# Optimization experiments

Hardware: AMD Instinct MI355X
Metric: run time of the kernel (lower is better)

Reference implementation:

```python
import jax, jax.numpy as jnp
import numpy as np


def setup_inputs() -> dict:
    key = jax.random.key(0)
    ks = jax.random.split(key, 8)
    B, M, N, F, H, O = 4, 4096, 4096, 8, 128, 8
    feat = jax.random.normal(ks[0], (B, N, F), dtype=jnp.float32)
    adj = jax.random.uniform(ks[1], (B, M, N), dtype=jnp.float32)
    # MLP params (Linear: y = x @ W.T + b), torch default-like scale
    def lin(k, fan_in, fan_out):
        lim = 1.0 / np.sqrt(fan_in)
        kw, kb = jax.random.split(k)
        W = jax.random.uniform(kw, (fan_out, fan_in), minval=-lim, maxval=lim, dtype=jnp.float32)
        b = jax.random.uniform(kb, (fan_out,), minval=-lim, maxval=lim, dtype=jnp.float32)
        return W, b
    W1, b1 = lin(ks[2], F, H)
    W2, b2 = lin(ks[3], H, H)
    W3, b3 = lin(ks[4], H, O)
    return {"feat": feat, "adj": adj, "W1": W1, "b1": b1, "W2": W2, "b2": b2, "W3": W3, "b3": b3}


def reference(feat, adj, W1, b1, W2, b2, W3, b3):
    # b = sum_n adj[..., m, n] * feat[..., n, f]  ==  adj @ feat
    b = jnp.einsum('bmn,bnf->bmf', adj, feat)  # [B, M, F]
    h = jax.nn.elu(b @ W1.T + b1)              # [B, M, H]
    h = jax.nn.elu(h @ W2.T + b2)              # [B, M, H]
    c = h @ W3.T + b3                          # [B, M, O]
    return c
```

## Files before the change

### kernel.cpp

```cpp
#include <hip/hip_runtime.h>
#include <cstdint>
#include <cstddef>

#define B_ 4
#define M_ 4096
#define N_ 4096
#define F_ 8
#define H_ 128
#define O_ 8

__device__ __forceinline__ uint32_t f2bf1(float x) {
    uint32_t u = __float_as_uint(x);
    return (u + 0x7fffu + ((u >> 16) & 1u)) >> 16;
}

__device__ __forceinline__ void bf8dec(uint4 w, float* f) {
    f[0] = __uint_as_float(w.x << 16);
    f[1] = __uint_as_float(w.x & 0xffff0000u);
    f[2] = __uint_as_float(w.y << 16);
    f[3] = __uint_as_float(w.y & 0xffff0000u);
    f[4] = __uint_as_float(w.z << 16);
    f[5] = __uint_as_float(w.z & 0xffff0000u);
    f[6] = __uint_as_float(w.w << 16);
    f[7] = __uint_as_float(w.w & 0xffff0000u);
}

__device__ __forceinline__ float elu(float x) {
    return x > 0.f ? x : (__expf(x) - 1.f);
}

typedef float vf4_t __attribute__((ext_vector_type(4)));
__device__ __forceinline__ float4 ntload4(const float4* p) {
    vf4_t v = __builtin_nontemporal_load((const vf4_t*)p);
    float4 r;
    r.x = v.x; r.y = v.y; r.z = v.z; r.w = v.w;
    return r;
}

__global__ __launch_bounds__(512, 4)
void k_fused(const float* __restrict__ adj, const float* __restrict__ feat,
             const float* __restrict__ W1, const float* __restrict__ b1,
             const float* __restrict__ W2, const float* __restrict__ b2,
             const float* __restrict__ W3, const float* __restrict__ b3,
             float* __restrict__ out) {
    __shared__ alignas(16) unsigned char smem[65536];
    uint4* sfeat = (uint4*)smem;
    float* sW1 = (float*)smem;
    float* sW3 = (float*)(smem + 4096);
    float* sB1 = (float*)(smem + 8320);
    float* sB2 = (float*)(smem + 8832);
    float* sB3 = (float*)(smem + 9344);
    float* sH  = (float*)(smem + 9376);
    unsigned short* sW2b = (unsigned short*)(smem + 26272);

    const int tid = threadIdx.x;
    const int bb  = blockIdx.x >> 7;
    const int rb  = blockIdx.x & 127;

    const float4* fsrc = (const float4*)(feat + (size_t)bb * (N_ * F_));
    for (int n = tid; n < N_; n += 512) {
        float4 lo = fsrc[2 * n];
        float4 hi = fsrc[2 * n + 1];
        uint4 w;
        w.x = f2bf1(lo.x) | (f2bf1(lo.y) << 16);
        w.y = f2bf1(lo.z) | (f2bf1(lo.w) << 16);
        w.z = f2bf1(hi.x) | (f2bf1(hi.y) << 16);
        w.w = f2bf1(hi.z) | (f2bf1(hi.w) << 16);
        sfeat[(n & 3) * 1024 + (n >> 2)] = w;
    }
    __syncthreads();

    const int lane = tid & 63;
    const int wv   = tid >> 6;
    const int m0   = rb * 32 + wv * 4;

    const float4* arow = (const float4*)(adj + (size_t)(bb * M_ + m0) * N_);

    float acc[4][8];
#pragma unroll
    for (int r = 0; r < 4; ++r)
#pragma unroll
        for (int f = 0; f < 8; ++f) acc[r][f] = 0.f;

    float4 na0 = ntload4(arow + lane);
    float4 na1 = ntload4(arow + lane + 1024);
    float4 na2 = ntload4(arow + lane + 2048);
    float4 na3 = ntload4(arow + lane + 3072);

#pragma unroll 1
    for (int c = 0; c < 16; ++c) {
        const int ni = (c << 6) + lane;
        float4 a0 = na0, a1 = na1, a2 = na2, a3 = na3;
        uint4 w0 = sfeat[ni];
        uint4 w1 = sfeat[1024 + ni];
        uint4 w2 = sfeat[2048 + ni];
        uint4 w3 = sfeat[3072 + ni];
        if (c < 15) {
            const int nn = ni + 64;
            na0 = ntload4(arow + nn);
            na1 = ntload4(arow + nn + 1024);
            na2 = ntload4(arow + nn + 2048);
            na3 = ntload4(arow + nn + 3072);
        }

        float av[4][4] = {{a0.x, a1.x, a2.x, a3.x},
                          {a0.y, a1.y, a2.y, a3.y},
                          {a0.z, a1.z, a2.z, a3.z},
                          {a0.w, a1.w, a2.w, a3.w}};
        uint4 ww[4] = {w0, w1, w2, w3};
#pragma unroll
        for (int k = 0; k < 4; ++k) {
            float f[8];
            bf8dec(ww[k], f);
#pragma unroll
            for (int r = 0; r < 4; ++r) {
                const float a = av[k][r];
#pragma unroll
                for (int j = 0; j < 8; ++j)
                    acc[r][j] = fmaf(a, f[j], acc[r][j]);
            }
        }
    }

#pragma unroll
    for (int r = 0; r < 4; ++r)
#pragma unroll
        for (int j = 0; j < 8; ++j) {
            float v = acc[r][j];
            v += __shfl_xor(v, 32, 64);
            v += __shfl_xor(v, 16, 64);
            v += __shfl_xor(v, 8, 64);
            v += __shfl_xor(v, 4, 64);
            v += __shfl_xor(v, 2, 64);
            v += __shfl_xor(v, 1, 64);
            acc[r][j] = v;
        }

    __syncthreads();

    for (int i = tid; i < H_ * F_ / 4; i += 512)
        ((float4*)sW1)[i] = ((const float4*)W1)[i];

    for (int i8 = tid; i8 < H_ * H_ / 8; i8 += 512) {
        const int idx = i8 * 8;
        const int o = idx >> 7, k = idx & 127;
        float4 lo = ((const float4*)W2)[i8 * 2];
        float4 hi = ((const float4*)W2)[i8 * 2 + 1];
        uint4 w;
        w.x = f2bf1(lo.x) | (f2bf1(lo.y) << 16);
        w.y = f2bf1(lo.z) | (f2bf1(lo.w) << 16);
        w.z = f2bf1(hi.x) | (f2bf1(hi.y) << 16);
        w.w = f2bf1(hi.z) | (f2bf1(hi.w) << 16);
        *((uint4*)&sW2b[o * 136 + k]) = w;
    }

    for (int i = tid; i < O_ * H_ / 4; i += 512) {
        const int idx = i * 4;
        const int o = idx >> 7, k = idx & 127;
        *((float4*)&sW3[o * 132 + k]) = ((const float4*)W3)[i];
    }
    if (tid < H_) { sB1[tid] = b1[tid]; sB2[tid] = b2[tid]; }
    if (tid < O_) sB3[tid] = b3[tid];
    __syncthreads();

    float w1a[8], w1b[8];
    {
        float4 x0 = *(const float4*)&sW1[lane * 8];
        float4 x1 = *(const float4*)&sW1[lane * 8 + 4];
        float4 y0 = *(const float4*)&sW1[(lane + 64) * 8];
        float4 y1 = *(const float4*)&sW1[(lane + 64) * 8 + 4];
        w1a[0]=x0.x; w1a[1]=x0.y; w1a[2]=x0.z; w1a[3]=x0.w;
        w1a[4]=x1.x; w1a[5]=x1.y; w1a[6]=x1.z; w1a[7]=x1.w;
        w1b[0]=y0.x; w1b[1]=y0.y; w1b[2]=y0.z; w1b[3]=y0.w;
        w1b[4]=y1.x; w1b[5]=y1.y; w1b[6]=y1.z; w1b[7]=y1.w;
    }
    const float bias1a = sB1[lane], bias1b = sB1[lane + 64];
#pragma unroll
    for (int r = 0; r < 4; ++r) {
        float t0 = bias1a, t1 = bias1b;
#pragma unroll
        for (int j = 0; j < 8; ++j) {
            t0 = fmaf(acc[r][j], w1a[j], t0);
            t1 = fmaf(acc[r][j], w1b[j], t1);
        }
        sH[(wv * 4 + r) * 132 + lane]      = elu(t0);
        sH[(wv * 4 + r) * 132 + lane + 64] = elu(t1);
    }

    float a20[4], a21[4];
#pragma unroll
    for (int r = 0; r < 4; ++r) { a20[r] = 0.f; a21[r] = 0.f; }
#pragma unroll 1
    for (int oct = 0; oct < 16; ++oct) {
        uint4 wa = *(const uint4*)&sW2b[lane * 136 + (oct << 3)];
        uint4 wb = *(const uint4*)&sW2b[(lane + 64) * 136 + (oct << 3)];
        float A[8], Bv[8];
        bf8dec(wa, A);
        bf8dec(wb, Bv);
#pragma unroll
        for (int r = 0; r < 4; ++r) {
            const float* hp = &sH[(wv * 4 + r) * 132 + (oct << 3)];
            float4 h0 = *(const float4*)hp;
            float4 h1v = *(const float4*)(hp + 4);
            float hv[8] = {h0.x, h0.y, h0.z, h0.w, h1v.x, h1v.y, h1v.z, h1v.w};
#pragma unroll
            for (int j = 0; j < 8; ++j) {
                a20[r] = fmaf(hv[j], A[j], a20[r]);
                a21[r] = fmaf(hv[j], Bv[j], a21[r]);
            }
        }
    }
    const float bias2a = sB2[lane], bias2b = sB2[lane + 64];
#pragma unroll
    for (int r = 0; r < 4; ++r) {
        sH[(wv * 4 + r) * 132 + lane]      = elu(a20[r] + bias2a);
        sH[(wv * 4 + r) * 132 + lane + 64] = elu(a21[r] + bias2b);
    }

    if (lane < 32) {
        const int rr = lane >> 3;
        const int oo = lane & 7;
        const float* hp = &sH[(wv * 4 + rr) * 132];
        const float* wp = &sW3[oo * 132];
        float s = sB3[oo];
#pragma unroll
        for (int k = 0; k < 128; k += 4) {
            float4 h = *(const float4*)(hp + k);
            float4 g = *(const float4*)(wp + k);
            s = fmaf(h.x, g.x, fmaf(h.y, g.y, fmaf(h.z, g.z, fmaf(h.w, g.w, s))));
        }
        out[(size_t)(bb * M_ + m0 + rr) * 8 + oo] = s;
    }
}

extern "C" void kernel_launch(void* const* d_in, const int* in_sizes, int n_in,
                              void* d_out, int out_size, void* d_ws, size_t ws_size,
                              hipStream_t stream) {
    const float* feat = (const float*)d_in[0];
    const float* adj  = (const float*)d_in[1];
    const float* W1   = (const float*)d_in[2];
    const float* b1   = (const float*)d_in[3];
    const float* W2   = (const float*)d_in[4];
    const float* b2   = (const float*)d_in[5];
    const float* W3   = (const float*)d_in[6];
    const float* b3   = (const float*)d_in[7];
    float* outp = (float*)d_out;

    k_fused<<<dim3(B_ * 128), dim3(512), 0, stream>>>(
        adj, feat, W1, b1, W2, b2, W3, b3, outp);
}
```

Baseline: 378.0 us.

## Prefetch MLP weights into registers before reduction and lower occupancy bound

The W1, bias, W2 and W3 global loads are issued right after the adjacency accumulation loop, so their latency overlaps the cross-lane shuffle reduction. W1 and the biases stay in registers instead of going through shared memory. W2 is converted to bf16 in registers and written to shared memory after the existing barrier. The barrier is moved to after the layer-1 sH writes, and launch_bounds is relaxed from 4 to 2 blocks per CU to give room for the extra live registers, which may reduce occupancy in the memory-bound main loop.

```diff
diff --git a/kernel.cpp b/kernel.cpp
--- a/kernel.cpp
+++ b/kernel.cpp
@@ -37,7 +37,7 @@
     return r;
 }
 
-__global__ __launch_bounds__(512, 4)
+__global__ __launch_bounds__(512, 2)
 void k_fused(const float* __restrict__ adj, const float* __restrict__ feat,
              const float* __restrict__ W1, const float* __restrict__ b1,
              const float* __restrict__ W2, const float* __restrict__ b2,
@@ -45,17 +45,16 @@
              float* __restrict__ out) {
     __shared__ alignas(16) unsigned char smem[65536];
     uint4* sfeat = (uint4*)smem;
-    float* sW1 = (float*)smem;
-    float* sW3 = (float*)(smem + 4096);
-    float* sB1 = (float*)(smem + 8320);
-    float* sB2 = (float*)(smem + 8832);
-    float* sB3 = (float*)(smem + 9344);
-    float* sH  = (float*)(smem + 9376);
-    unsigned short* sW2b = (unsigned short*)(smem + 26272);
-
-    const int tid = threadIdx.x;
-    const int bb  = blockIdx.x >> 7;
-    const int rb  = blockIdx.x & 127;
+    float* sW3 = (float*)smem;
+    float* sH  = (float*)(smem + 4224);
+    unsigned short* sW2b = (unsigned short*)(smem + 21120);
+
+    const int tid  = threadIdx.x;
+    const int bb   = blockIdx.x >> 7;
+    const int rb   = blockIdx.x & 127;
+    const int lane = tid & 63;
+    const int wv   = tid >> 6;
+    const int m0   = rb * 32 + wv * 4;
 
     const float4* fsrc = (const float4*)(feat + (size_t)bb * (N_ * F_));
     for (int n = tid; n < N_; n += 512) {
@@ -69,10 +68,6 @@
         sfeat[(n & 3) * 1024 + (n >> 2)] = w;
     }
     __syncthreads();
-
-    const int lane = tid & 63;
-    const int wv   = tid >> 6;
-    const int m0   = rb * 32 + wv * 4;
 
     const float4* arow = (const float4*)(adj + (size_t)(bb * M_ + m0) * N_);
 
@@ -122,6 +117,23 @@
         }
     }
 
+    float4 x0 = *(const float4*)&W1[lane * 8];
+    float4 x1 = *(const float4*)&W1[lane * 8 + 4];
+    float4 y0 = *(const float4*)&W1[(lane + 64) * 8];
+    float4 y1 = *(const float4*)&W1[(lane + 64) * 8 + 4];
+    const float bias1a = b1[lane], bias1b = b1[lane + 64];
+    const float bias2a = b2[lane], bias2b = b2[lane + 64];
+    float b3v = (lane < 32) ? b3[lane & 7] : 0.f;
+    float4 w2lo[4], w2hi[4];
+#pragma unroll
+    for (int g = 0; g < 4; ++g) {
+        const int i8 = tid + g * 512;
+        w2lo[g] = ((const float4*)W2)[2 * i8];
+        w2hi[g] = ((const float4*)W2)[2 * i8 + 1];
+    }
+    float4 w3v = make_float4(0.f, 0.f, 0.f, 0.f);
+    if (tid < 256) w3v = ((const float4*)W3)[tid];
+
 #pragma unroll
     for (int r = 0; r < 4; ++r)
 #pragma unroll
@@ -136,45 +148,35 @@
             acc[r][j] = v;
         }
 
+    uint4 w2p[4];
+#pragma unroll
+    for (int g = 0; g < 4; ++g) {
+        uint4 w;
+        w.x = f2bf1(w2lo[g].x) | (f2bf1(w2lo[g].y) << 16);
+        w.y = f2bf1(w2lo[g].z) | (f2bf1(w2lo[g].w) << 16);
+        w.z = f2bf1(w2hi[g].x) | (f2bf1(w2hi[g].y) << 16);
+        w.w = f2bf1(w2hi[g].z) | (f2bf1(w2hi[g].w) << 16);
+        w2p[g] = w;
+    }
+
     __syncthreads();
 
-    for (int i = tid; i < H_ * F_ / 4; i += 512)
-        ((float4*)sW1)[i] = ((const float4*)W1)[i];
-
-    for (int i8 = tid; i8 < H_ * H_ / 8; i8 += 512) {
-        const int idx = i8 * 8;
+#pragma unroll
+    for (int g = 0; g < 4; ++g) {
+        const int idx = (tid + g * 512) * 8;
         const int o = idx >> 7, k = idx & 127;
-        float4 lo = ((const float4*)W2)[i8 * 2];
-        float4 hi = ((const float4*)W2)[i8 * 2 + 1];
-        uint4 w;
-        w.x = f2bf1(lo.x) | (f2bf1(lo.y) << 16);
-        w.y = f2bf1(lo.z) | (f2bf1(lo.w) << 16);
-        w.z = f2bf1(hi.x) | (f2bf1(hi.y) << 16);
-        w.w = f2bf1(hi.z) | (f2bf1(hi.w) << 16);
-        *((uint4*)&sW2b[o * 136 + k]) = w;
-    }
-
-    for (int i = tid; i < O_ * H_ / 4; i += 512) {
-        const int idx = i * 4;
-        const int o = idx >> 7, k = idx & 127;
-        *((float4*)&sW3[o * 132 + k]) = ((const float4*)W3)[i];
-    }
-    if (tid < H_) { sB1[tid] = b1[tid]; sB2[tid] = b2[tid]; }
-    if (tid < O_) sB3[tid] = b3[tid];
-    __syncthreads();
+        *((uint4*)&sW2b[o * 136 + k]) = w2p[g];
+    }
+    if (tid < 256) {
+        const int idx = tid * 4;
+        *((float4*)&sW3[(idx >> 7) * 132 + (idx & 127)]) = w3v;
+    }
 
     float w1a[8], w1b[8];
-    {
-        float4 x0 = *(const float4*)&sW1[lane * 8];
-        float4 x1 = *(const float4*)&sW1[lane * 8 + 4];
-        float4 y0 = *(const float4*)&sW1[(lane + 64) * 8];
-        float4 y1 = *(const float4*)&sW1[(lane + 64) * 8 + 4];
-        w1a[0]=x0.x; w1a[1]=x0.y; w1a[2]=x0.z; w1a[3]=x0.w;
-        w1a[4]=x1.x; w1a[5]=x1.y; w1a[6]=x1.z; w1a[7]=x1.w;
-        w1b[0]=y0.x; w1b[1]=y0.y; w1b[2]=y0.z; w1b[3]=y0.w;
-        w1b[4]=y1.x; w1b[5]=y1.y; w1b[6]=y1.z; w1b[7]=y1.w;
-    }
-    const float bias1a = sB1[lane], bias1b = sB1[lane + 64];
+    w1a[0]=x0.x; w1a[1]=x0.y; w1a[2]=x0.z; w1a[3]=x0.w;
+    w1a[4]=x1.x; w1a[5]=x1.y; w1a[6]=x1.z; w1a[7]=x1.w;
+    w1b[0]=y0.x; w1b[1]=y0.y; w1b[2]=y0.z; w1b[3]=y0.w;
+    w1b[4]=y1.x; w1b[5]=y1.y; w1b[6]=y1.z; w1b[7]=y1.w;
 #pragma unroll
     for (int r = 0; r < 4; ++r) {
         float t0 = bias1a, t1 = bias1b;
@@ -186,6 +188,8 @@
         sH[(wv * 4 + r) * 132 + lane]      = elu(t0);
         sH[(wv * 4 + r) * 132 + lane + 64] = elu(t1);
     }
+
+    __syncthreads();
 
     float a20[4], a21[4];
 #pragma unroll
@@ -210,7 +214,6 @@
             }
         }
     }
-    const float bias2a = sB2[lane], bias2b = sB2[lane + 64];
 #pragma unroll
     for (int r = 0; r < 4; ++r) {
         sH[(wv * 4 + r) * 132 + lane]      = elu(a20[r] + bias2a);
@@ -222,7 +225,7 @@
         const int oo = lane & 7;
         const float* hp = &sH[(wv * 4 + rr) * 132];
         const float* wp = &sW3[oo * 132];
-        float s = sB3[oo];
+        float s = b3v;
 #pragma unroll
         for (int k = 0; k < 128; k += 4) {
             float4 h = *(const float4*)(hp + k);
```

New measurement: 384.5 us. About the same (+1.7%).
